# Kernel optimization log

Hardware: AMD Instinct MI355X
Metric: run time of the kernel (lower is better)

The kernel has to match this reference:

```python
import jax, jax.numpy as jnp
import numpy as np

N = 50000      # nodes
E = 600000     # edges
IN = 128       # in_channels
HID = 128      # GCN hidden width (fixed in module)
H = 4          # TransformerConv heads
C = 32         # out_channels per head (heads*C = 128)


def _lin(k, fan_in, fan_out):
    return jax.random.normal(k, (fan_in, fan_out), jnp.float32) / np.sqrt(fan_in)


def setup_inputs() -> dict:
    key = jax.random.key(0)
    ks = jax.random.split(key, 12)
    return {
        "x": jax.random.normal(ks[0], (N, IN), jnp.float32),
        "edge_index": jax.random.randint(ks[1], (2, E), 0, N, dtype=jnp.int32),
        "W_gcn": _lin(ks[2], IN, HID),
        "b_gcn": jnp.zeros((HID,), jnp.float32),
        "Wq": _lin(ks[3], HID, H * C),
        "bq": jnp.zeros((H * C,), jnp.float32),
        "Wk": _lin(ks[4], HID, H * C),
        "bk": jnp.zeros((H * C,), jnp.float32),
        "Wv": _lin(ks[5], HID, H * C),
        "bv": jnp.zeros((H * C,), jnp.float32),
        "Ws": _lin(ks[6], HID, H * C),
        "bs": jnp.zeros((H * C,), jnp.float32),
    }


def reference(x, edge_index, W_gcn, b_gcn, Wq, bq, Wk, bk, Wv, bv, Ws, bs):
    n = x.shape[0]
    idt = edge_index.dtype

    # ---- GCNConv: x' = D^{-1/2}(A+I)D^{-1/2} x W + b, then ReLU ----
    h = x @ W_gcn                                   # [N, HID] linear first (PyG order)
    loop = jnp.arange(n, dtype=idt)
    src = jnp.concatenate([edge_index[0], loop])    # with self-loops
    tgt = jnp.concatenate([edge_index[1], loop])
    deg = jax.ops.segment_sum(jnp.ones(src.shape, h.dtype), tgt, num_segments=n)
    dinv = jnp.where(deg > 0, jax.lax.rsqrt(deg), 0.0)
    norm = dinv[src] * dinv[tgt]                    # [E+N]
    h = jax.ops.segment_sum(h[src] * norm[:, None], tgt, num_segments=n)
    h = jax.nn.relu(h + b_gcn)                      # [N, HID]

    # ---- TransformerConv (heads=4, concat=True, no self-loops added) ----
    s, t = edge_index[0], edge_index[1]
    q = (h @ Wq + bq).reshape(n, H, C)
    k = (h @ Wk + bk).reshape(n, H, C)
    v = (h @ Wv + bv).reshape(n, H, C)

    alpha = jnp.einsum('ehc,ehc->eh', q[t], k[s]) / np.sqrt(C)   # [E, H]
    m = jax.lax.stop_gradient(jax.ops.segment_max(alpha, t, num_segments=n))
    ea = jnp.exp(alpha - m[t])
    denom = jax.ops.segment_sum(ea, t, num_segments=n)           # [N, H]
    w = ea / jnp.where(denom[t] > 0, denom[t], 1.0)              # softmax per target node

    out = jax.ops.segment_sum(w[:, :, None] * v[s], t, num_segments=n)  # [N, H, C]
    out = out.reshape(n, H * C)

    # root/skip connection (lin_skip)
    return out + h @ Ws + bs
```

## Files before the change

### kernel.cpp

```cpp
#include <hip/hip_runtime.h>
#include <hip/hip_bf16.h>

typedef __attribute__((ext_vector_type(8))) short short8;
typedef __attribute__((ext_vector_type(4))) float floatx4;
typedef _Float16 half2v __attribute__((ext_vector_type(2)));

__device__ __forceinline__ float ld_f(const void* p, int f32, int i) {
  if (f32) return ((const float*)p)[i];
  unsigned short u = ((const unsigned short*)p)[i];
  return __uint_as_float(((unsigned)u) << 16);
}
__device__ __forceinline__ short ld_bf(const void* p, int f32, int i) {
  if (!f32) return ((const short*)p)[i];
  __hip_bfloat16 h = __float2bfloat16(((const float*)p)[i]);
  return *reinterpret_cast<short*>(&h);
}
__device__ __forceinline__ unsigned short f_to_bfu(float v) {
  __hip_bfloat16 h = __float2bfloat16(v);
  return *reinterpret_cast<unsigned short*>(&h);
}
__device__ __forceinline__ short f_to_h(float v) {
  _Float16 h = (_Float16)v;
  return *reinterpret_cast<short*>(&h);
}
__device__ __forceinline__ float bflo(unsigned w) { return __uint_as_float(w << 16); }
__device__ __forceinline__ float bfhi(unsigned w) { return __uint_as_float(w & 0xFFFF0000u); }

__global__ void init_kernel(const unsigned short* __restrict__ xs, int* __restrict__ flag,
                            int* __restrict__ cnt, int N) {
  if (blockIdx.x == 0) {
    __shared__ int sbad;
    if (threadIdx.x == 0) sbad = 0;
    __syncthreads();
    int bad = 0;
    for (int j = 2 * threadIdx.x; j < 16384; j += 512) {
      unsigned e = (xs[j] >> 7) & 0xFF;
      if (e >= 0xF0) bad = 1;
    }
    if (bad) atomicOr(&sbad, 1);
    __syncthreads();
    if (threadIdx.x == 0) flag[0] = sbad;
    return;
  }
  int i = (blockIdx.x - 1) * blockDim.x + threadIdx.x;
  if (i < N) cnt[i] = 0;
}

__global__ void prep_hist(const void* bg, const void* bq, const void* bk, const void* bv,
                          const void* bs, const void* Wg, const void* Wq, const void* Wk,
                          const void* Wv, const void* Ws, const int* __restrict__ flag,
                          float* __restrict__ bgf, float* __restrict__ bias512,
                          short* __restrict__ WpG, short* __restrict__ WpQ,
                          const int* __restrict__ ei, int* __restrict__ cnt,
                          int* __restrict__ erank, int E, int Gp) {
  if ((int)blockIdx.x >= Gp) {
    int e = (blockIdx.x - Gp) * blockDim.x + threadIdx.x;
    if (e < E) erank[e] = atomicAdd(&cnt[ei[E + e]], 1);
    return;
  }
  int tid = blockIdx.x * blockDim.x + threadIdx.x;
  int f = *flag;
  if (tid < 128) { bgf[tid] = ld_f(bg, f, tid); return; }
  if (tid < 640) {
    int t = tid - 128;
    const void* b = (t < 128) ? bq : (t < 256) ? bk : (t < 384) ? bv : bs;
    bias512[t] = ld_f(b, f, t & 127);
    return;
  }
  if (tid < 640 + 2048) {
    int id = tid - 640;
    int lane = id & 63, kb = (id >> 6) & 3, tn = id >> 8;
    int k0 = kb * 32 + (lane >> 4) * 8;
    int n = tn * 16 + (lane & 15);
    short* dst = WpG + (size_t)id * 8;
#pragma unroll
    for (int j = 0; j < 8; ++j) dst[j] = ld_bf(Wg, f, (k0 + j) * 128 + n);
    return;
  }
  if (tid < 640 + 2048 + 8192) {
    int id = tid - 640 - 2048;
    int lane = id & 63, kb = (id >> 6) & 3, tn = id >> 8;
    int k0 = kb * 32 + (lane >> 4) * 8;
    int n = tn * 16 + (lane & 15);
    const void* W = (n < 128) ? Wq : (n < 256) ? Wk : (n < 384) ? Wv : Ws;
    int col = n & 127;
    short* dst = WpQ + (size_t)id * 8;
#pragma unroll
    for (int j = 0; j < 8; ++j) dst[j] = ld_bf(W, f, (k0 + j) * 128 + col);
  }
}

__global__ void scanA(const int* __restrict__ cnt, int* __restrict__ chunkscan,
                      int* __restrict__ partials, int N) {
  __shared__ int sh[1024];
  int t = threadIdx.x;
  int g = blockIdx.x * 1024 + t;
  int v = (g < N) ? cnt[g] : 0;
  sh[t] = v;
  __syncthreads();
  for (int o = 1; o < 1024; o <<= 1) {
    int add = (t >= o) ? sh[t - o] : 0;
    __syncthreads();
    sh[t] += add;
    __syncthreads();
  }
  if (g < N) chunkscan[g] = sh[t];
  if (t == 1023) partials[blockIdx.x] = sh[1023];
}

__global__ void scanB(int* __restrict__ partials, int nb) {
  int lane = threadIdx.x;
  if (nb <= 64) {
    int v = (lane < nb) ? partials[lane] : 0;
#pragma unroll
    for (int o = 1; o < 64; o <<= 1) {
      int t = __shfl_up(v, o);
      if (lane >= o) v += t;
    }
    int ex = __shfl_up(v, 1);
    if (lane == 0) ex = 0;
    if (lane < nb) partials[lane] = ex;
    return;
  }
  if (lane == 0) {
    int run = 0;
    for (int b = 0; b < nb; ++b) {
      int t = partials[b];
      partials[b] = run;
      run += t;
    }
  }
}

__global__ void scanC(const int* __restrict__ cnt, const int* __restrict__ chunkscan,
                      const int* __restrict__ partials, int* __restrict__ rowptr,
                      float* __restrict__ dinv, int N) {
  int g = blockIdx.x * blockDim.x + threadIdx.x;
  if (g == 0) rowptr[0] = 0;
  if (g >= N) return;
  int c = cnt[g];
  int inc = chunkscan[g] + partials[g >> 10];
  rowptr[g + 1] = inc;
  dinv[g] = rsqrtf((float)c + 1.0f);
}

__global__ void gemmh0_fill(const void* __restrict__ X, const int* __restrict__ flag,
                            const short* __restrict__ Bp, const float* __restrict__ dinv,
                            short* __restrict__ C, int M, const int* __restrict__ ei,
                            const int* __restrict__ rowptr, const int* __restrict__ erank,
                            int* __restrict__ srcs, int E, int Gg) {
  if ((int)blockIdx.x >= Gg) {
    int e = (blockIdx.x - Gg) * blockDim.x + threadIdx.x;
    if (e < E) {
      int t = ei[E + e];
      srcs[rowptr[t] + erank[e]] = ei[e];
    }
    return;
  }
  int wv = (blockIdx.x * blockDim.x + threadIdx.x) >> 6;
  int lane = threadIdx.x & 63;
  int tilesM = (M + 15) >> 4;
  if (wv >= tilesM) return;
  int f = *flag;
  int tm = wv;
  int m = tm * 16 + (lane & 15);
  int mc = m < M ? m : M - 1;
  int quad = lane >> 4;
  short8 a[4];
  if (f) {
    const float4* xr = (const float4*)((const float*)X + (size_t)mc * 128) + quad * 2;
#pragma unroll
    for (int kb = 0; kb < 4; ++kb) {
      float4 u = xr[kb * 8];
      float4 w = xr[kb * 8 + 1];
      a[kb][0] = (short)f_to_bfu(u.x);
      a[kb][1] = (short)f_to_bfu(u.y);
      a[kb][2] = (short)f_to_bfu(u.z);
      a[kb][3] = (short)f_to_bfu(u.w);
      a[kb][4] = (short)f_to_bfu(w.x);
      a[kb][5] = (short)f_to_bfu(w.y);
      a[kb][6] = (short)f_to_bfu(w.z);
      a[kb][7] = (short)f_to_bfu(w.w);
    }
  } else {
    const short* xr = (const short*)X + (size_t)mc * 128 + quad * 8;
#pragma unroll
    for (int kb = 0; kb < 4; ++kb) a[kb] = *(const short8*)(xr + kb * 32);
  }
  floatx4 acc[8];
#pragma unroll
  for (int tn = 0; tn < 8; ++tn) acc[tn] = (floatx4){0.f, 0.f, 0.f, 0.f};
#pragma unroll
  for (int kb = 0; kb < 4; ++kb) {
#pragma unroll
    for (int tn = 0; tn < 8; ++tn) {
      short8 b8 = *(const short8*)(Bp + ((size_t)(tn * 4 + kb) * 64 + lane) * 8);
      acc[tn] = __builtin_amdgcn_mfma_f32_16x16x32_bf16(a[kb], b8, acc[tn], 0, 0, 0);
    }
  }
  int row0 = tm * 16 + quad * 4;
  int cl = lane & 15;
  float dsc[4];
#pragma unroll
  for (int r = 0; r < 4; ++r) dsc[r] = (row0 + r < M) ? dinv[row0 + r] : 0.f;
#pragma unroll
  for (int tn = 0; tn < 8; ++tn)
#pragma unroll
    for (int r = 0; r < 4; ++r)
      if (row0 + r < M)
        C[(size_t)(row0 + r) * 128 + tn * 16 + cl] = (short)f_to_bfu(acc[tn][r] * dsc[r]);
}

__global__ void gcn_gather(const int* __restrict__ rowptr, const int* __restrict__ srcs,
                           const float* __restrict__ dinv, const unsigned* __restrict__ h0,
                           const float* __restrict__ bgf, unsigned* __restrict__ hbf, int N) {
  int wv = (int)((blockIdx.x * (long long)blockDim.x + threadIdx.x) >> 6);
  int lane = threadIdx.x & 63;
  int hf = lane >> 5, q2 = (lane >> 4) & 1, sl = lane & 15, sl32 = lane & 31;
  int node = wv * 2 + hf;
  int nodec = node < N ? node : N - 1;
  int beg = rowptr[nodec], end = rowptr[nodec + 1];
  int deg = node < N ? end - beg : 0;
  int dm1 = deg - 1;
  int dmc = dm1 > 0 ? dm1 : 0;
  int sreg = srcs[deg > 0 ? beg + (sl32 < dm1 ? sl32 : dm1) : 0];
  int degmax = deg;
  degmax = max(degmax, __shfl_xor(degmax, 32));
  int dd = degmax < 32 ? degmax : 32;
  int hb = hf << 5;
  float a0 = 0.f, a1 = 0.f, a2 = 0.f, a3 = 0.f, a4 = 0.f, a5 = 0.f, a6 = 0.f, a7 = 0.f;
  for (int base = 0; base < dd; base += 8) {
    int p0 = base + q2, p1 = p0 + 2, p2 = p0 + 4, p3 = p0 + 6;
    int s0 = __shfl(sreg, hb + (p0 < dmc ? p0 : dmc));
    int s1 = __shfl(sreg, hb + (p1 < dmc ? p1 : dmc));
    int s2 = __shfl(sreg, hb + (p2 < dmc ? p2 : dmc));
    int s3 = __shfl(sreg, hb + (p3 < dmc ? p3 : dmc));
    float m0 = p0 < deg ? 1.f : 0.f;
    float m1 = p1 < deg ? 1.f : 0.f;
    float m2 = p2 < deg ? 1.f : 0.f;
    float m3 = p3 < deg ? 1.f : 0.f;
    uint4 w0 = *(const uint4*)(h0 + (size_t)s0 * 64 + sl * 4);
    uint4 w1 = *(const uint4*)(h0 + (size_t)s1 * 64 + sl * 4);
    uint4 w2 = *(const uint4*)(h0 + (size_t)s2 * 64 + sl * 4);
    uint4 w3 = *(const uint4*)(h0 + (size_t)s3 * 64 + sl * 4);
    a0 += m0 * bflo(w0.x) + m1 * bflo(w1.x) + m2 * bflo(w2.x) + m3 * bflo(w3.x);
    a1 += m0 * bfhi(w0.x) + m1 * bfhi(w1.x) + m2 * bfhi(w2.x) + m3 * bfhi(w3.x);
    a2 += m0 * bflo(w0.y) + m1 * bflo(w1.y) + m2 * bflo(w2.y) + m3 * bflo(w3.y);
    a3 += m0 * bfhi(w0.y) + m1 * bfhi(w1.y) + m2 * bfhi(w2.y) + m3 * bfhi(w3.y);
    a4 += m0 * bflo(w0.z) + m1 * bflo(w1.z) + m2 * bflo(w2.z) + m3 * bflo(w3.z);
    a5 += m0 * bfhi(w0.z) + m1 * bfhi(w1.z) + m2 * bfhi(w2.z) + m3 * bfhi(w3.z);
    a6 += m0 * bflo(w0.w) + m1 * bflo(w1.w) + m2 * bflo(w2.w) + m3 * bflo(w3.w);
    a7 += m0 * bfhi(w0.w) + m1 * bfhi(w1.w) + m2 * bfhi(w2.w) + m3 * bfhi(w3.w);
  }
  for (int i = beg + 32 + q2; i < end; i += 2) {
    uint4 w0 = *(const uint4*)(h0 + (size_t)srcs[i] * 64 + sl * 4);
    a0 += bflo(w0.x);
    a1 += bfhi(w0.x);
    a2 += bflo(w0.y);
    a3 += bfhi(w0.y);
    a4 += bflo(w0.z);
    a5 += bfhi(w0.z);
    a6 += bflo(w0.w);
    a7 += bfhi(w0.w);
  }
  a0 += __shfl_xor(a0, 16);
  a1 += __shfl_xor(a1, 16);
  a2 += __shfl_xor(a2, 16);
  a3 += __shfl_xor(a3, 16);
  a4 += __shfl_xor(a4, 16);
  a5 += __shfl_xor(a5, 16);
  a6 += __shfl_xor(a6, 16);
  a7 += __shfl_xor(a7, 16);
  if (q2 == 0 && node < N) {
    uint4 hw = *(const uint4*)(h0 + (size_t)node * 64 + sl * 4);
    float dt = dinv[node];
    const float4* bb = (const float4*)bgf;
    float4 b0 = bb[sl * 2], b1 = bb[sl * 2 + 1];
    float v0 = (a0 + bflo(hw.x)) * dt + b0.x;
    float v1 = (a1 + bfhi(hw.x)) * dt + b0.y;
    float v2 = (a2 + bflo(hw.y)) * dt + b0.z;
    float v3 = (a3 + bfhi(hw.y)) * dt + b0.w;
    float v4 = (a4 + bflo(hw.z)) * dt + b1.x;
    float v5 = (a5 + bfhi(hw.z)) * dt + b1.y;
    float v6 = (a6 + bflo(hw.w)) * dt + b1.z;
    float v7 = (a7 + bfhi(hw.w)) * dt + b1.w;
    v0 = v0 > 0.f ? v0 : 0.f;
    v1 = v1 > 0.f ? v1 : 0.f;
    v2 = v2 > 0.f ? v2 : 0.f;
    v3 = v3 > 0.f ? v3 : 0.f;
    v4 = v4 > 0.f ? v4 : 0.f;
    v5 = v5 > 0.f ? v5 : 0.f;
    v6 = v6 > 0.f ? v6 : 0.f;
    v7 = v7 > 0.f ? v7 : 0.f;
    uint4 o;
    o.x = (unsigned)f_to_bfu(v0) | ((unsigned)f_to_bfu(v1) << 16);
    o.y = (unsigned)f_to_bfu(v2) | ((unsigned)f_to_bfu(v3) << 16);
    o.z = (unsigned)f_to_bfu(v4) | ((unsigned)f_to_bfu(v5) << 16);
    o.w = (unsigned)f_to_bfu(v6) | ((unsigned)f_to_bfu(v7) << 16);
    *(uint4*)(hbf + (size_t)node * 64 + sl * 4) = o;
  }
}

__global__ void gemm_qkvs(const short* __restrict__ A, const short* __restrict__ Bp,
                          const float* __restrict__ bias512, short* __restrict__ qb,
                          short* __restrict__ kvb, short* __restrict__ skipb, int M) {
  int wv = (blockIdx.x * blockDim.x + threadIdx.x) >> 6;
  int lane = threadIdx.x & 63;
  int tilesM = (M + 15) >> 4;
  if (wv >= tilesM * 4) return;
  int tng = wv & 3, tm = wv >> 2;
  int m = tm * 16 + (lane & 15);
  int mc = m < M ? m : M - 1;
  int quad = lane >> 4;
  const short* Arow = A + (size_t)mc * 128 + quad * 8;
  short8 a[4];
#pragma unroll
  for (int kb = 0; kb < 4; ++kb) a[kb] = *(const short8*)(Arow + kb * 32);
  floatx4 acc[8];
#pragma unroll
  for (int j = 0; j < 8; ++j) acc[j] = (floatx4){0.f, 0.f, 0.f, 0.f};
#pragma unroll
  for (int kb = 0; kb < 4; ++kb) {
#pragma unroll
    for (int j = 0; j < 8; ++j) {
      int tn = tng * 8 + j;
      short8 b8 = *(const short8*)(Bp + ((size_t)(tn * 4 + kb) * 64 + lane) * 8);
      acc[j] = __builtin_amdgcn_mfma_f32_16x16x32_bf16(a[kb], b8, acc[j], 0, 0, 0);
    }
  }
  int row0 = tm * 16 + quad * 4;
  int cl = lane & 15;
#pragma unroll
  for (int j = 0; j < 8; ++j) {
    int cc = j * 16 + cl;
    float b = bias512[tng * 128 + cc];
#pragma unroll
    for (int r = 0; r < 4; ++r) {
      int row = row0 + r;
      if (row >= M) continue;
      float val = acc[j][r] + b;
      if (tng == 0) {
        qb[(size_t)row * 128 + cc] = f_to_h(val);
      } else if (tng == 3) {
        skipb[(size_t)row * 128 + cc] = (short)f_to_bfu(val);
      } else {
        size_t base = (size_t)row * 256 + (size_t)((cc >> 2) * 8 + (cc & 3));
        if (tng == 1)
          kvb[base] = f_to_h(val);
        else
          kvb[base + 4] = (short)f_to_bfu(val);
      }
    }
  }
}

__device__ __forceinline__ float dpp_red8(float p) {
  p += __int_as_float(__builtin_amdgcn_mov_dpp(__float_as_int(p), 0xB1, 0xF, 0xF, true));
  p += __int_as_float(__builtin_amdgcn_mov_dpp(__float_as_int(p), 0x4E, 0xF, 0xF, true));
  p += __int_as_float(__builtin_amdgcn_mov_dpp(__float_as_int(p), 0x141, 0xF, 0xF, true));
  return p;
}
__device__ __forceinline__ float dot_dpp(half2v qa, half2v qc, unsigned kw0, unsigned kw1) {
  half2v k0 = *reinterpret_cast<half2v*>(&kw0);
  half2v k1 = *reinterpret_cast<half2v*>(&kw1);
#if __has_builtin(__builtin_amdgcn_fdot2)
  float p = __builtin_amdgcn_fdot2(qa, k0, 0.f, false);
  p = __builtin_amdgcn_fdot2(qc, k1, p, false);
#else
  float p = (float)qa[0] * (float)k0[0] + (float)qa[1] * (float)k0[1] +
            (float)qc[0] * (float)k1[0] + (float)qc[1] * (float)k1[1];
#endif
  return dpp_red8(p) * 0.17677669529663687f;
}

__global__ void attn_fused(const int* __restrict__ rowptr, const int* __restrict__ srcs,
                           const unsigned* __restrict__ qb, const unsigned* __restrict__ kvb,
                           const unsigned* __restrict__ skipb, float* __restrict__ out, int N) {
  int wv = (int)((blockIdx.x * (long long)blockDim.x + threadIdx.x) >> 6);
  int lane = threadIdx.x & 63;
  int hf = lane >> 5, sl = lane & 31;
  int node = wv * 2 + hf;
  int nodec = node < N ? node : N - 1;
  uint2 qw = *(const uint2*)(qb + (size_t)nodec * 64 + sl * 2);
  half2v qa = *reinterpret_cast<half2v*>(&qw.x);
  half2v qc = *reinterpret_cast<half2v*>(&qw.y);
  int beg = rowptr[nodec], end = rowptr[nodec + 1];
  int deg = node < N ? end - beg : 0;
  int dm1 = deg - 1;
  int dmc = dm1 > 0 ? dm1 : 0;
  int sreg = srcs[deg > 0 ? beg + (sl < dm1 ? sl : dm1) : 0];
  int degmax = deg;
  degmax = max(degmax, __shfl_xor(degmax, 32));
  int dd = degmax < 32 ? degmax : 32;
  int hb = hf << 5;

  float denom = 0.f, ax0 = 0.f, ax1 = 0.f, ax2 = 0.f, ax3 = 0.f;
  for (int base = 0; base < dd; base += 4) {
    int p0 = base, p1 = base + 1, p2 = base + 2, p3 = base + 3;
    int s0 = __shfl(sreg, hb + (p0 < dmc ? p0 : dmc));
    int s1 = __shfl(sreg, hb + (p1 < dmc ? p1 : dmc));
    int s2 = __shfl(sreg, hb + (p2 < dmc ? p2 : dmc));
    int s3 = __shfl(sreg, hb + (p3 < dmc ? p3 : dmc));
    uint4 kv0 = *(const uint4*)(kvb + (size_t)s0 * 128 + sl * 4);
    uint4 kv1 = *(const uint4*)(kvb + (size_t)s1 * 128 + sl * 4);
    uint4 kv2 = *(const uint4*)(kvb + (size_t)s2 * 128 + sl * 4);
    uint4 kv3 = *(const uint4*)(kvb + (size_t)s3 * 128 + sl * 4);
    float e0 = __expf(dot_dpp(qa, qc, kv0.x, kv0.y));
    float e1 = __expf(dot_dpp(qa, qc, kv1.x, kv1.y));
    float e2 = __expf(dot_dpp(qa, qc, kv2.x, kv2.y));
    float e3 = __expf(dot_dpp(qa, qc, kv3.x, kv3.y));
    e0 = p0 < deg ? e0 : 0.f;
    e1 = p1 < deg ? e1 : 0.f;
    e2 = p2 < deg ? e2 : 0.f;
    e3 = p3 < deg ? e3 : 0.f;
    denom += e0 + e1 + e2 + e3;
    ax0 += e0 * bflo(kv0.z) + e1 * bflo(kv1.z) + e2 * bflo(kv2.z) + e3 * bflo(kv3.z);
    ax1 += e0 * bfhi(kv0.z) + e1 * bfhi(kv1.z) + e2 * bfhi(kv2.z) + e3 * bfhi(kv3.z);
    ax2 += e0 * bflo(kv0.w) + e1 * bflo(kv1.w) + e2 * bflo(kv2.w) + e3 * bflo(kv3.w);
    ax3 += e0 * bfhi(kv0.w) + e1 * bfhi(kv1.w) + e2 * bfhi(kv2.w) + e3 * bfhi(kv3.w);
  }
  for (int i = beg + 32; i < end; ++i) {
    int s0 = srcs[i];
    uint4 kv0 = *(const uint4*)(kvb + (size_t)s0 * 128 + sl * 4);
    float e0 = __expf(dot_dpp(qa, qc, kv0.x, kv0.y));
    denom += e0;
    ax0 += e0 * bflo(kv0.z);
    ax1 += e0 * bfhi(kv0.z);
    ax2 += e0 * bflo(kv0.w);
    ax3 += e0 * bfhi(kv0.w);
  }
  if (node < N) {
    float r = denom > 0.f ? 1.f / denom : 0.f;
    uint2 sw = *(const uint2*)(skipb + (size_t)node * 64 + sl * 2);
    float4 o;
    o.x = ax0 * r + bflo(sw.x);
    o.y = ax1 * r + bfhi(sw.x);
    o.z = ax2 * r + bflo(sw.y);
    o.w = ax3 * r + bfhi(sw.y);
    *(float4*)(out + (size_t)node * 128 + sl * 4) = o;
  }
}

extern "C" void kernel_launch(void* const* d_in, const int* in_sizes, int n_in,
                              void* d_out, int out_size, void* d_ws, size_t ws_size,
                              hipStream_t stream) {
  const void* x  = d_in[0];
  const int* ei  = (const int*)d_in[1];
  const void* Wg = d_in[2];
  const void* bg = d_in[3];
  const void* Wq = d_in[4];
  const void* bq = d_in[5];
  const void* Wk = d_in[6];
  const void* bk = d_in[7];
  const void* Wv = d_in[8];
  const void* bv = d_in[9];
  const void* Ws = d_in[10];
  const void* bs = d_in[11];
  float* out = (float*)d_out;

  const int N = in_sizes[0] / 128;
  const int E = in_sizes[1] / 2;
  int tilesM = (N + 15) / 16;
  int nscan = (N + 1023) / 1024;
  const int B = 256;

  char* ws = (char*)d_ws;
  size_t off = 0;
  auto carve = [&](size_t bytes) -> void* {
    void* p = ws + off;
    off += (bytes + 255) & ~(size_t)255;
    return p;
  };
  int* flag = (int*)carve(256);
  float* bias512 = (float*)carve(512 * 4);
  float* bgf = (float*)carve(128 * 4);
  float* dinv = (float*)carve((size_t)N * 4);
  int* cnt = (int*)carve((size_t)N * 4);
  int* rowptr = (int*)carve((size_t)(N + 1) * 4);
  int* chunkscan = (int*)carve((size_t)N * 4);
  int* partials = (int*)carve((size_t)(nscan + 1) * 4);
  int* srcs = (int*)carve((size_t)E * 4);
  int* erank = (int*)carve((size_t)E * 4);
  short* WpG = (short*)carve((size_t)16384 * 2);
  short* WpQ = (short*)carve((size_t)65536 * 2);
  short* h0bf = (short*)carve((size_t)N * 128 * 2);
  short* hbf = (short*)carve((size_t)N * 128 * 2);
  short* qb = (short*)carve((size_t)N * 128 * 2);
  short* kvb = (short*)carve((size_t)N * 256 * 2);
  short* skipb = (short*)carve((size_t)N * 128 * 2);

  int Gp = (10880 + B - 1) / B;
  int Gh = (E + B - 1) / B;
  int Gg = (tilesM * 64 + B - 1) / B;
  int Gf = (E + B - 1) / B;

  init_kernel<<<1 + (N + B - 1) / B, B, 0, stream>>>((const unsigned short*)x, flag, cnt, N);
  prep_hist<<<Gp + Gh, B, 0, stream>>>(bg, bq, bk, bv, bs, Wg, Wq, Wk, Wv, Ws, flag,
                                       bgf, bias512, WpG, WpQ, ei, cnt, erank, E, Gp);
  scanA<<<nscan, 1024, 0, stream>>>(cnt, chunkscan, partials, N);
  scanB<<<1, 64, 0, stream>>>(partials, nscan);
  scanC<<<(N + B - 1) / B, B, 0, stream>>>(cnt, chunkscan, partials, rowptr, dinv, N);
  gemmh0_fill<<<Gg + Gf, B, 0, stream>>>(x, flag, WpG, dinv, h0bf, N, ei, rowptr, erank,
                                         srcs, E, Gg);
  gcn_gather<<<(N + 7) / 8, B, 0, stream>>>(rowptr, srcs, dinv, (const unsigned*)h0bf, bgf,
                                            (unsigned*)hbf, N);
  gemm_qkvs<<<(tilesM * 4 + 3) / 4, B, 0, stream>>>(hbf, WpQ, bias512, qb, kvb, skipb, N);
  attn_fused<<<(N + 7) / 8, B, 0, stream>>>(rowptr, srcs, (const unsigned*)qb,
                                            (const unsigned*)kvb, (const unsigned*)skipb, out, N);
}
```

Measured before the change: 260.8 us.

## Assign one node per wavefront in attention, splitting edges across half-waves

The attention kernel now gives each target node a full 64-lane wave. The two 32-lane halves process alternating edges, and their partial softmax sums are merged with cross-half shuffles. The main loop issues 8 independent KV gathers per half before computing, to raise memory-level parallelism and stop wasting lanes on degree imbalance between paired nodes. The cost is twice as many waves, extra shuffles at the end, and more padded work for low-degree nodes (average degree is about 12).

```diff
diff --git a/kernel.cpp b/kernel.cpp
--- a/kernel.cpp
+++ b/kernel.cpp
@@ -376,50 +376,43 @@
 __global__ void attn_fused(const int* __restrict__ rowptr, const int* __restrict__ srcs,
                            const unsigned* __restrict__ qb, const unsigned* __restrict__ kvb,
                            const unsigned* __restrict__ skipb, float* __restrict__ out, int N) {
-  int wv = (int)((blockIdx.x * (long long)blockDim.x + threadIdx.x) >> 6);
+  int node = (int)((blockIdx.x * (long long)blockDim.x + threadIdx.x) >> 6);
+  if (node >= N) return;
   int lane = threadIdx.x & 63;
   int hf = lane >> 5, sl = lane & 31;
-  int node = wv * 2 + hf;
-  int nodec = node < N ? node : N - 1;
-  uint2 qw = *(const uint2*)(qb + (size_t)nodec * 64 + sl * 2);
+  uint2 qw = *(const uint2*)(qb + (size_t)node * 64 + sl * 2);
   half2v qa = *reinterpret_cast<half2v*>(&qw.x);
   half2v qc = *reinterpret_cast<half2v*>(&qw.y);
-  int beg = rowptr[nodec], end = rowptr[nodec + 1];
-  int deg = node < N ? end - beg : 0;
+  int beg = rowptr[node], end = rowptr[node + 1];
+  int deg = end - beg;
   int dm1 = deg - 1;
   int dmc = dm1 > 0 ? dm1 : 0;
-  int sreg = srcs[deg > 0 ? beg + (sl < dm1 ? sl : dm1) : 0];
-  int degmax = deg;
-  degmax = max(degmax, __shfl_xor(degmax, 32));
-  int dd = degmax < 32 ? degmax : 32;
-  int hb = hf << 5;
+  int sreg = srcs[deg > 0 ? beg + (lane < dm1 ? lane : dm1) : 0];
+  int dd = deg < 64 ? deg : 64;
 
   float denom = 0.f, ax0 = 0.f, ax1 = 0.f, ax2 = 0.f, ax3 = 0.f;
-  for (int base = 0; base < dd; base += 4) {
-    int p0 = base, p1 = base + 1, p2 = base + 2, p3 = base + 3;
-    int s0 = __shfl(sreg, hb + (p0 < dmc ? p0 : dmc));
-    int s1 = __shfl(sreg, hb + (p1 < dmc ? p1 : dmc));
-    int s2 = __shfl(sreg, hb + (p2 < dmc ? p2 : dmc));
-    int s3 = __shfl(sreg, hb + (p3 < dmc ? p3 : dmc));
-    uint4 kv0 = *(const uint4*)(kvb + (size_t)s0 * 128 + sl * 4);
-    uint4 kv1 = *(const uint4*)(kvb + (size_t)s1 * 128 + sl * 4);
-    uint4 kv2 = *(const uint4*)(kvb + (size_t)s2 * 128 + sl * 4);
-    uint4 kv3 = *(const uint4*)(kvb + (size_t)s3 * 128 + sl * 4);
-    float e0 = __expf(dot_dpp(qa, qc, kv0.x, kv0.y));
-    float e1 = __expf(dot_dpp(qa, qc, kv1.x, kv1.y));
-    float e2 = __expf(dot_dpp(qa, qc, kv2.x, kv2.y));
-    float e3 = __expf(dot_dpp(qa, qc, kv3.x, kv3.y));
-    e0 = p0 < deg ? e0 : 0.f;
-    e1 = p1 < deg ? e1 : 0.f;
-    e2 = p2 < deg ? e2 : 0.f;
-    e3 = p3 < deg ? e3 : 0.f;
-    denom += e0 + e1 + e2 + e3;
-    ax0 += e0 * bflo(kv0.z) + e1 * bflo(kv1.z) + e2 * bflo(kv2.z) + e3 * bflo(kv3.z);
-    ax1 += e0 * bfhi(kv0.z) + e1 * bfhi(kv1.z) + e2 * bfhi(kv2.z) + e3 * bfhi(kv3.z);
-    ax2 += e0 * bflo(kv0.w) + e1 * bflo(kv1.w) + e2 * bflo(kv2.w) + e3 * bflo(kv3.w);
-    ax3 += e0 * bfhi(kv0.w) + e1 * bfhi(kv1.w) + e2 * bfhi(kv2.w) + e3 * bfhi(kv3.w);
-  }
-  for (int i = beg + 32; i < end; ++i) {
+  for (int base = 0; base < dd; base += 16) {
+    uint4 kv[8];
+    int pp[8];
+#pragma unroll
+    for (int j = 0; j < 8; ++j) {
+      int p = base + hf + 2 * j;
+      pp[j] = p;
+      int s = __shfl(sreg, p < dmc ? p : dmc);
+      kv[j] = *(const uint4*)(kvb + (size_t)s * 128 + sl * 4);
+    }
+#pragma unroll
+    for (int j = 0; j < 8; ++j) {
+      float e = __expf(dot_dpp(qa, qc, kv[j].x, kv[j].y));
+      e = pp[j] < deg ? e : 0.f;
+      denom += e;
+      ax0 += e * bflo(kv[j].z);
+      ax1 += e * bfhi(kv[j].z);
+      ax2 += e * bflo(kv[j].w);
+      ax3 += e * bfhi(kv[j].w);
+    }
+  }
+  for (int i = beg + 64 + hf; i < end; i += 2) {
     int s0 = srcs[i];
     uint4 kv0 = *(const uint4*)(kvb + (size_t)s0 * 128 + sl * 4);
     float e0 = __expf(dot_dpp(qa, qc, kv0.x, kv0.y));
@@ -429,7 +422,12 @@
     ax2 += e0 * bflo(kv0.w);
     ax3 += e0 * bfhi(kv0.w);
   }
-  if (node < N) {
+  denom += __shfl_xor(denom, 32);
+  ax0 += __shfl_xor(ax0, 32);
+  ax1 += __shfl_xor(ax1, 32);
+  ax2 += __shfl_xor(ax2, 32);
+  ax3 += __shfl_xor(ax3, 32);
+  if (hf == 0) {
     float r = denom > 0.f ? 1.f / denom : 0.f;
     uint2 sw = *(const uint2*)(skipb + (size_t)node * 64 + sl * 2);
     float4 o;
@@ -505,6 +503,6 @@
   gcn_gather<<<(N + 7) / 8, B, 0, stream>>>(rowptr, srcs, dinv, (const unsigned*)h0bf, bgf,
                                             (unsigned*)hbf, N);
   gemm_qkvs<<<(tilesM * 4 + 3) / 4, B, 0, stream>>>(hbf, WpQ, bias512, qb, kvb, skipb, N);
-  attn_fused<<<(N + 7) / 8, B, 0, stream>>>(rowptr, srcs, (const unsigned*)qb,
+  attn_fused<<<(N + 3) / 4, B, 0, stream>>>(rowptr, srcs, (const unsigned*)qb,
                                             (const unsigned*)kvb, (const unsigned*)skipb, out, N);
 }
```

Result: no change. 263.7 us (+1.1%).
